# Kernel optimization log

Measured on AMD Instinct MI355X. Metric: run time of the kernel, lower is better.

The kernel has to match this reference:

```python
import jax, jax.numpy as jnp
import numpy as np

CHEB_K = 3  # from init_kwargs

def _layernorm(v, g, b, eps=1e-12):
    mu = jnp.mean(v, axis=-1, keepdims=True)
    var = jnp.var(v, axis=-1, keepdims=True)  # biased, matches torch LayerNorm
    return (v - mu) * jax.lax.rsqrt(var + eps) * g + b

def setup_inputs() -> dict:
    key = jax.random.key(0)
    ks = jax.random.split(key, 5)
    B, N, D_IN, D_OUT, E = 64, 2048, 64, 64, 16
    return {
        "x": jax.random.normal(ks[0], (B, N, D_IN), dtype=jnp.float32),
        "node_embeddings": jax.random.normal(ks[1], (N, E), dtype=jnp.float32),
        "time_embeddings": jax.random.normal(ks[2], (E,), dtype=jnp.float32),
        "weights_pool": jax.random.normal(ks[3], (E, CHEB_K, D_IN, D_OUT), dtype=jnp.float32) * 0.1,
        "bias_pool": jax.random.normal(ks[4], (E, D_OUT), dtype=jnp.float32) * 0.1,
        "ln_gamma": jnp.ones((E,), dtype=jnp.float32),
        "ln_beta": jnp.zeros((E,), dtype=jnp.float32),
    }

def reference(x, node_embeddings, time_embeddings, weights_pool, bias_pool, ln_gamma, ln_beta):
    N = node_embeddings.shape[0]
    # dropout in eval mode -> identity
    ne = _layernorm(node_embeddings + time_embeddings[None, :], ln_gamma, ln_beta)  # [N,E]
    supports0 = jax.nn.softmax(ne @ ne.T, axis=1)  # [N,N]
    support_set = [jnp.eye(N, dtype=x.dtype), supports0]
    for _ in range(2, CHEB_K):
        support_set.append(2.0 * supports0 @ support_set[-1] - support_set[-2])
    supports = jnp.stack(support_set, axis=0)  # [K,N,N]
    weights = jnp.einsum('nd,dkio->nkio', ne, weights_pool)  # [N,K,I,O]
    bias = ne @ bias_pool  # [N,O]
    x_g = jnp.einsum('knm,bmc->bnkc', supports, x)  # [B,N,K,I]
    return jnp.einsum('bnki,nkio->bno', x_g, weights) + bias  # [B,N,O]
```

## Files before the change

### kernel.cpp

```cpp
#include <hip/hip_runtime.h>
#include <stdint.h>

typedef unsigned short u16;
typedef __attribute__((ext_vector_type(8))) short   bf16x8;
typedef __attribute__((ext_vector_type(4))) float   f32x4;
typedef __attribute__((ext_vector_type(4))) u16     u16x4;
typedef __attribute__((ext_vector_type(8))) u16     u16x8;

#define NN 2048
#define BB 64
#define DD 64
#define XSTRIDE (NN*DD)

__device__ __forceinline__ float bf2f(u16 u) {
    union { unsigned int i; float f; } v; v.i = ((unsigned int)u) << 16; return v.f;
}
__device__ __forceinline__ u16 f2bf(float f) {
    union { float f; unsigned int i; } v; v.f = f;
    unsigned int u = v.i;
    return (u16)((u + 0x7fffu + ((u >> 16) & 1u)) >> 16);
}

typedef __attribute__((address_space(3))) unsigned int lds_u32_t;
typedef const __attribute__((address_space(1))) unsigned int g_u32_t;
__device__ __forceinline__ void gload_lds16(const void* g, void* l) {
    __builtin_amdgcn_global_load_lds((g_u32_t*)(uintptr_t)g, (lds_u32_t*)(uintptr_t)l, 16, 0, 0);
}

__global__ __launch_bounds__(256) void k_ln(const float* __restrict__ nodee,
                                            const float* __restrict__ timee,
                                            const float* __restrict__ gamma,
                                            const float* __restrict__ beta,
                                            float* __restrict__ ne,
                                            u16* __restrict__ neb) {
    int n = blockIdx.x * 256 + threadIdx.x;
    float v[16]; float mu = 0.f;
    const float4* p = (const float4*)(nodee + (long)n * 16);
#pragma unroll
    for (int i = 0; i < 4; i++) {
        float4 q = p[i];
        v[i*4+0]=q.x; v[i*4+1]=q.y; v[i*4+2]=q.z; v[i*4+3]=q.w;
    }
#pragma unroll
    for (int e = 0; e < 16; e++) { v[e] += timee[e]; mu += v[e]; }
    mu *= (1.f/16.f);
    float var = 0.f;
#pragma unroll
    for (int e = 0; e < 16; e++) { float d = v[e]-mu; var += d*d; }
    var *= (1.f/16.f);
    float rs = rsqrtf(var + 1e-12f);
    float4* o = (float4*)(ne + (long)n * 16);
    u16x8 nb[2];
#pragma unroll
    for (int i = 0; i < 4; i++) {
        float4 q;
        q.x = (v[i*4+0]-mu)*rs*gamma[i*4+0] + beta[i*4+0];
        q.y = (v[i*4+1]-mu)*rs*gamma[i*4+1] + beta[i*4+1];
        q.z = (v[i*4+2]-mu)*rs*gamma[i*4+2] + beta[i*4+2];
        q.w = (v[i*4+3]-mu)*rs*gamma[i*4+3] + beta[i*4+3];
        o[i] = q;
        nb[i>>1][(i&1)*4+0] = f2bf(q.x); nb[i>>1][(i&1)*4+1] = f2bf(q.y);
        nb[i>>1][(i&1)*4+2] = f2bf(q.z); nb[i>>1][(i&1)*4+3] = f2bf(q.w);
    }
    u16x8 z;
#pragma unroll
    for (int j = 0; j < 8; j++) z[j] = 0;
    u16x8* ob = (u16x8*)&neb[(long)n * 32];
    ob[0] = nb[0]; ob[1] = nb[1]; ob[2] = z; ob[3] = z;
}

__global__ __launch_bounds__(256) void k_wperm(const float* __restrict__ wp,
                                               u16* __restrict__ wpP) {
    int j = blockIdx.x * 256 + threadIdx.x;
    int o = j / 192, ki = j - o * 192;
    int src = ki * 64 + o;
    u16x8 ov[4];
#pragma unroll
    for (int e = 0; e < 16; e++) ov[e>>3][e&7] = f2bf(wp[(long)e*12288 + src]);
#pragma unroll
    for (int e = 0; e < 8; e++) { ov[2][e] = 0; ov[3][e] = 0; }
    u16x8* dst = (u16x8*)&wpP[(long)j * 32];
    dst[0]=ov[0]; dst[1]=ov[1]; dst[2]=ov[2]; dst[3]=ov[3];
}

__global__ __launch_bounds__(256) void k_softmax(const float* __restrict__ ne,
                                                 u16* __restrict__ S) {
    __shared__ float row[2048];
    __shared__ float red[8];
    int n = blockIdx.x, t = threadIdx.x;
    int wave = t >> 6, lane = t & 63;
    f32x4 nev[4];
#pragma unroll
    for (int i = 0; i < 4; i++) nev[i] = *(const f32x4*)&ne[n*16 + i*4];
    float lmax = -1e30f;
    for (int m = t; m < 2048; m += 256) {
        const f32x4* p = (const f32x4*)&ne[m*16];
        f32x4 d4 = nev[0]*p[0] + nev[1]*p[1] + nev[2]*p[2] + nev[3]*p[3];
        float d = d4[0]+d4[1]+d4[2]+d4[3];
        row[m] = d;
        lmax = fmaxf(lmax, d);
    }
#pragma unroll
    for (int off = 32; off > 0; off >>= 1) lmax = fmaxf(lmax, __shfl_xor(lmax, off));
    if (lane == 0) red[wave] = lmax;
    __syncthreads();
    float gmax = fmaxf(fmaxf(red[0], red[1]), fmaxf(red[2], red[3]));
    float lsum = 0.f;
    for (int m = t; m < 2048; m += 256) {
        float ev = __expf(row[m] - gmax);
        row[m] = ev;
        lsum += ev;
    }
#pragma unroll
    for (int off = 32; off > 0; off >>= 1) lsum += __shfl_xor(lsum, off);
    __syncthreads();
    if (lane == 0) red[wave] = lsum;
    __syncthreads();
    float inv = 1.f / (red[0]+red[1]+red[2]+red[3]);
    for (int m = t; m < 2048; m += 256)
        S[(long)n*2048 + m] = f2bf(row[m] * inv);
}

__global__ __launch_bounds__(256) void k_permute(const float* __restrict__ x,
                                                 u16* __restrict__ Xpt) {
    __shared__ u16 T[64][72];
    int bid = blockIdx.x;
    int b = bid >> 5, m0 = (bid & 31) * 64;
    int t = threadIdx.x;
#pragma unroll
    for (int it = 0; it < 4; it++) {
        int fi = it*256 + t;
        int row = fi >> 4, c4 = (fi & 15) * 4;
        float4 v = *(const float4*)&x[(long)b*XSTRIDE + (m0+row)*64 + c4];
        T[c4+0][row] = f2bf(v.x); T[c4+1][row] = f2bf(v.y);
        T[c4+2][row] = f2bf(v.z); T[c4+3][row] = f2bf(v.w);
    }
    __syncthreads();
#pragma unroll
    for (int it = 0; it < 2; it++) {
        int ch = it*256 + t;
        int c = ch >> 3, m8 = (ch & 7) * 8;
        u16x8 v = *(const u16x8*)&T[c][m8];
        *(u16x8*)&Xpt[(long)(b*64 + c)*2048 + m0 + m8] = v;
    }
}

__global__ __launch_bounds__(256) void k_gemm_bt(const u16* __restrict__ A,
                                                 const u16* __restrict__ Bt,
                                                 u16* __restrict__ C,
                                                 int M, int Ncols, int K) {
    __shared__ __align__(16) u16 As[128*32];
    __shared__ __align__(16) u16 Bs[128*32];
    const int t = threadIdx.x;
    const int wave = t >> 6, lane = t & 63;
    const int l15 = lane & 15, lhi = lane >> 4;
    const int m0 = blockIdx.y * 128;
    const int n0 = blockIdx.x * 128;
    const int wr = wave >> 1, wc = wave & 1;
    f32x4 acc[4][4] = {};
    const int srow = t >> 2;
    const int sk = (t & 3) * 8;
    const u16* gA = A + (long)(m0 + srow) * K + sk;
    const u16* gB = Bt + (long)(n0 + srow) * K + sk;
    const long half = (long)64 * K;
    u16* lA = As + wave * 512;
    u16* lB = Bs + wave * 512;
    const int aoff = (wr*64 + l15)*32 + lhi*8;
    const int boff = (wc*64 + l15)*32 + lhi*8;
    for (int k0 = 0; k0 < K; k0 += 32) {
        gload_lds16(gA + k0,        lA);
        gload_lds16(gA + k0 + half, lA + 2048);
        gload_lds16(gB + k0,        lB);
        gload_lds16(gB + k0 + half, lB + 2048);
        __syncthreads();
        bf16x8 af[4], bv[4];
#pragma unroll
        for (int m = 0; m < 4; m++) af[m] = *(const bf16x8*)&As[aoff + m*512];
#pragma unroll
        for (int q = 0; q < 4; q++) bv[q] = *(const bf16x8*)&Bs[boff + q*512];
#pragma unroll
        for (int m = 0; m < 4; m++)
#pragma unroll
            for (int q = 0; q < 4; q++)
                acc[m][q] = __builtin_amdgcn_mfma_f32_16x16x32_bf16(af[m], bv[q], acc[m][q], 0, 0, 0);
        __syncthreads();
    }
#pragma unroll
    for (int m = 0; m < 4; m++) {
        int row = m0 + wr*64 + m*16 + lhi*4;
#pragma unroll
        for (int q = 0; q < 4; q++) {
            int col = n0 + wc*64 + q*16 + l15;
#pragma unroll
            for (int r = 0; r < 4; r++)
                C[(long)(row + r) * Ncols + col] = f2bf(acc[m][q][r]);
        }
    }
}

__global__ __launch_bounds__(512, 1) void k_gemm_big(const u16* __restrict__ A,
                                                     const u16* __restrict__ Bt,
                                                     u16* __restrict__ C,
                                                     int M, int Ncols, int K) {
    __shared__ __align__(16) u16 As0[3 * 128 * 64];
    __shared__ __align__(16) u16 Bs0[3 * 256 * 64];
    const int t = threadIdx.x;
    const int wave = t >> 6, lane = t & 63;
    const int l15 = lane & 15, lhi = lane >> 4;
    const int nwg = gridDim.x * gridDim.y;
    const int wgid = blockIdx.y * gridDim.x + blockIdx.x;
    const int swz = (wgid & 7) * (nwg >> 3) + (wgid >> 3);
    const int by = swz / gridDim.x, bx = swz - (swz / gridDim.x) * gridDim.x;
    const int m0 = by * 128, n0 = bx * 256;
    const int wr = wave >> 2, wc = wave & 3;
    const int NT = K >> 6;
    f32x4 acc[4][4] = {};

    const u16* gAsrc[2];
#pragma unroll
    for (int r = 0; r < 2; r++) {
        int c = r*512 + t, row = c >> 3, slot = c & 7;
        gAsrc[r] = A + (long)(m0 + row) * K + ((slot ^ (row & 7)) * 8);
    }
    const u16* gBsrc[4];
#pragma unroll
    for (int r = 0; r < 4; r++) {
        int c = r*512 + t, row = c >> 3, slot = c & 7;
        gBsrc[r] = Bt + (long)(n0 + row) * K + ((slot ^ (row & 7)) * 8);
    }
    const int ldsA = wave * 512;
    const int ldsB = wave * 512;

    int curA = 0, nxtA = 8192,  tgtA = 16384;
    int curB = 0, nxtB = 16384, tgtB = 32768;

#pragma unroll
    for (int r = 0; r < 2; r++) gload_lds16(gAsrc[r],      &As0[curA + r*4096 + ldsA]);
#pragma unroll
    for (int r = 0; r < 4; r++) gload_lds16(gBsrc[r],      &Bs0[curB + r*4096 + ldsB]);
#pragma unroll
    for (int r = 0; r < 2; r++) gload_lds16(gAsrc[r] + 64, &As0[nxtA + r*4096 + ldsA]);
#pragma unroll
    for (int r = 0; r < 4; r++) gload_lds16(gBsrc[r] + 64, &Bs0[nxtB + r*4096 + ldsB]);
    asm volatile("s_waitcnt vmcnt(6)" ::: "memory");
    __builtin_amdgcn_s_barrier();
    asm volatile("" ::: "memory");

    const int rsw = l15 & 7;
    const int sw0 = (lhi ^ rsw) * 8;
    const int sw1 = ((4 + lhi) ^ rsw) * 8;
    const int aBase = (wr*64 + l15) * 64;
    const int bBase = (wc*64 + l15) * 64;

#pragma unroll 1
    for (int tt = 0; tt < NT; tt++) {
        const bool stg = (tt + 2 < NT);
        const int ko2 = (tt + 2) << 6;
        bf16x8 af0[4], bv0[4];
#pragma unroll
        for (int m = 0; m < 4; m++) af0[m] = *(const bf16x8*)&As0[curA + aBase + m*1024 + sw0];
#pragma unroll
        for (int q = 0; q < 4; q++) bv0[q] = *(const bf16x8*)&Bs0[curB + bBase + q*1024 + sw0];
        if (stg) {
            gload_lds16(gAsrc[0] + ko2, &As0[tgtA + 0*4096 + ldsA]);
            gload_lds16(gAsrc[1] + ko2, &As0[tgtA + 1*4096 + ldsA]);
            gload_lds16(gBsrc[0] + ko2, &Bs0[tgtB + 0*4096 + ldsB]);
        }
        __builtin_amdgcn_s_setprio(1);
#pragma unroll
        for (int m = 0; m < 4; m++)
#pragma unroll
            for (int q = 0; q < 4; q++)
                acc[m][q] = __builtin_amdgcn_mfma_f32_16x16x32_bf16(af0[m], bv0[q], acc[m][q], 0, 0, 0);
        __builtin_amdgcn_s_setprio(0);
        bf16x8 af1[4], bv1[4];
#pragma unroll
        for (int m = 0; m < 4; m++) af1[m] = *(const bf16x8*)&As0[curA + aBase + m*1024 + sw1];
#pragma unroll
        for (int q = 0; q < 4; q++) bv1[q] = *(const bf16x8*)&Bs0[curB + bBase + q*1024 + sw1];
        if (stg) {
            gload_lds16(gBsrc[1] + ko2, &Bs0[tgtB + 1*4096 + ldsB]);
            gload_lds16(gBsrc[2] + ko2, &Bs0[tgtB + 2*4096 + ldsB]);
            gload_lds16(gBsrc[3] + ko2, &Bs0[tgtB + 3*4096 + ldsB]);
        }
        __builtin_amdgcn_s_setprio(1);
#pragma unroll
        for (int m = 0; m < 4; m++)
#pragma unroll
            for (int q = 0; q < 4; q++)
                acc[m][q] = __builtin_amdgcn_mfma_f32_16x16x32_bf16(af1[m], bv1[q], acc[m][q], 0, 0, 0);
        __builtin_amdgcn_s_setprio(0);
        asm volatile("" ::: "memory");
        if (stg)                asm volatile("s_waitcnt vmcnt(6)" ::: "memory");
        else if (tt + 1 < NT)   asm volatile("s_waitcnt vmcnt(0)" ::: "memory");
        if (tt + 1 < NT) {
            __builtin_amdgcn_s_barrier();
            asm volatile("" ::: "memory");
        }
        int ta = curA; curA = nxtA; nxtA = tgtA; tgtA = ta;
        int tb = curB; curB = nxtB; nxtB = tgtB; tgtB = tb;
    }
#pragma unroll
    for (int m = 0; m < 4; m++) {
        int row = m0 + wr*64 + m*16 + lhi*4;
#pragma unroll
        for (int q = 0; q < 4; q++) {
            int col = n0 + wc*64 + q*16 + l15;
#pragma unroll
            for (int r = 0; r < 4; r++)
                C[(long)(row + r) * Ncols + col] = f2bf(acc[m][q][r]);
        }
    }
}

__global__ __launch_bounds__(256) void k_transpose(const u16* __restrict__ in,
                                                   u16* __restrict__ out,
                                                   int R, int Ccols) {
    __shared__ __align__(16) u16 T[64][72];
    int r0 = blockIdx.y * 64, c0 = blockIdx.x * 64;
    int t = threadIdx.x;
#pragma unroll
    for (int it = 0; it < 2; it++) {
        int lin = it*2048 + t*8;
        int r = lin >> 6, c8 = lin & 63;
        u16x8 v = *(const u16x8*)&in[(long)(r0+r)*Ccols + c0 + c8];
        *(u16x8*)&T[r][c8] = v;
    }
    __syncthreads();
#pragma unroll
    for (int it = 0; it < 2; it++) {
        int lin = it*2048 + t*8;
        int c = lin >> 6, r8 = lin & 63;
        u16x8 v;
#pragma unroll
        for (int j = 0; j < 8; j++) v[j] = T[r8+j][c];
        *(u16x8*)&out[(long)(c0+c)*R + r0 + r8] = v;
    }
}

__global__ __launch_bounds__(256) void k_final(const float* __restrict__ x,
                                               const u16* __restrict__ Y1,
                                               const u16* __restrict__ Y2,
                                               const u16* __restrict__ Wt,
                                               const float* __restrict__ ne,
                                               const float* __restrict__ bp,
                                               float* __restrict__ out) {
    __shared__ __align__(16) u16 Al[64*200];
    __shared__ __align__(16) u16 Wl[64*200];
    __shared__ float biasl[64];
    int n = blockIdx.x;
    int t = threadIdx.x;
    int wave = t >> 6, lane = t & 63;
    int l15 = lane & 15, lhi = lane >> 4;
#pragma unroll
    for (int it = 0; it < 6; it++) {
        int ch = it*256 + t;
        int o = ch / 24, kl = (ch % 24) * 8;
        u16x8 v = *(const u16x8*)&Wt[(long)n*12288 + ch*8];
        *(u16x8*)&Wl[o*200 + kl] = v;
    }
    float xs[16];
#pragma unroll
    for (int it = 0; it < 4; it++) {
        int fi = it*256 + t;
        int b = fi >> 4, i4 = (fi & 15) * 4;
        float4 v = *(const float4*)&x[(long)b*XSTRIDE + n*64 + i4];
        xs[it*4+0]=v.x; xs[it*4+1]=v.y; xs[it*4+2]=v.z; xs[it*4+3]=v.w;
        u16x4 p; p[0]=f2bf(v.x); p[1]=f2bf(v.y); p[2]=f2bf(v.z); p[3]=f2bf(v.w);
        *(u16x4*)&Al[b*200 + i4] = p;
    }
#pragma unroll
    for (int it = 0; it < 2; it++) {
        int ch = it*256 + t;
        int b = ch >> 3, i8 = (ch & 7)*8;
        u16x8 v = *(const u16x8*)&Y1[(long)n*4096 + ch*8];
        *(u16x8*)&Al[b*200 + 64 + i8] = v;
    }
#pragma unroll
    for (int it = 0; it < 4; it++) {
        int fi = it*256 + t;
        int b = fi >> 4, i4 = (fi & 15)*4;
        u16x4 y = *(const u16x4*)&Y2[(long)n*4096 + fi*4];
        u16x4 p;
#pragma unroll
        for (int j = 0; j < 4; j++) p[j] = f2bf(2.f*bf2f(y[j]) - xs[it*4+j]);
        *(u16x4*)&Al[b*200 + 128 + i4] = p;
    }
    if (t < 64) {
        float s = 0.f;
#pragma unroll
        for (int e = 0; e < 16; e++) s += ne[n*16+e] * bp[e*64 + t];
        biasl[t] = s;
    }
    __syncthreads();
    f32x4 acc[4] = {};
#pragma unroll
    for (int kk = 0; kk < 6; kk++) {
        bf16x8 bv = *(const bf16x8*)&Wl[(wave*16 + l15)*200 + kk*32 + lhi*8];
#pragma unroll
        for (int m = 0; m < 4; m++) {
            bf16x8 av = *(const bf16x8*)&Al[(m*16 + l15)*200 + kk*32 + lhi*8];
            acc[m] = __builtin_amdgcn_mfma_f32_16x16x32_bf16(av, bv, acc[m], 0, 0, 0);
        }
    }
    int o = wave*16 + l15;
    float bias = biasl[o];
#pragma unroll
    for (int m = 0; m < 4; m++) {
        int brow = m*16 + lhi*4;
#pragma unroll
        for (int r = 0; r < 4; r++)
            out[(long)(brow + r)*XSTRIDE + n*64 + o] = acc[m][r] + bias;
    }
}

extern "C" void kernel_launch(void* const* d_in, const int* in_sizes, int n_in,
                              void* d_out, int out_size, void* d_ws, size_t ws_size,
                              hipStream_t stream) {
    const float* x     = (const float*)d_in[0];
    const float* nodee = (const float*)d_in[1];
    const float* timee = (const float*)d_in[2];
    const float* wp    = (const float*)d_in[3];
    const float* bp    = (const float*)d_in[4];
    const float* gamma = (const float*)d_in[5];
    const float* beta  = (const float*)d_in[6];
    float* out = (float*)d_out;

    char* ws = (char*)d_ws;
    float* ne  = (float*)(ws);
    u16* S     = (u16*)(ws + 131072);
    u16* Xpt   = (u16*)(ws + 8519680);
    u16* Y1    = (u16*)(ws + 25296896);
    u16* Y1t   = (u16*)(ws + 42074112);
    u16* Y2    = (u16*)(ws + 58851328);
    u16* Wt    = (u16*)(ws + 75628544);
    u16* neb   = (u16*)(ws + 58851328);
    u16* wpP   = (u16*)(ws + 58851328 + 131072);
    if (ws_size < (size_t)125960192) return;

    k_ln      <<<8,    256, 0, stream>>>(nodee, timee, gamma, beta, ne, neb);
    k_wperm   <<<48,   256, 0, stream>>>(wp, wpP);
    k_gemm_bt <<<dim3(96,16), 256, 0, stream>>>(neb, wpP, Wt, 2048, 12288, 32);
    k_softmax <<<2048, 256, 0, stream>>>(ne, S);
    k_permute <<<2048, 256, 0, stream>>>(x, Xpt);
    k_gemm_big<<<dim3(16,16), 512, 0, stream>>>(S, Xpt, Y1, 2048, 4096, 2048);
    k_transpose<<<dim3(64,32), 256, 0, stream>>>(Y1, Y1t, 2048, 4096);
    k_gemm_big<<<dim3(16,16), 512, 0, stream>>>(S, Y1t, Y2, 2048, 4096, 2048);
    k_final   <<<2048, 256, 0, stream>>>(x, Y1, Y2, Wt, ne, bp, out);
}
```

Measured before the change: 155.1 us.

## Fuse transpose into GEMM epilogue and switch big GEMM to four waves

The big GEMM goes from 8 waves of 64x64 tiles to 4 waves each computing 64x128, doubling accumulators per wave and reloading operands with the same swizzled LDS layout. The first GEMM also writes a transposed copy of its output through LDS in the epilogue, so the separate transpose kernel and its extra read of Y1 are gone. The intent is to cut a kernel launch plus a memory pass, and to raise MFMA work per LDS read. The cost is much higher register pressure (128 accumulator floats per lane) and fewer waves to hide latency.

```diff
diff --git a/kernel.cpp b/kernel.cpp
--- a/kernel.cpp
+++ b/kernel.cpp
@@ -198,12 +198,12 @@
     }
 }
 
-__global__ __launch_bounds__(512, 1) void k_gemm_big(const u16* __restrict__ A,
+__global__ __launch_bounds__(256, 1) void k_gemm_big(const u16* __restrict__ A,
                                                      const u16* __restrict__ Bt,
                                                      u16* __restrict__ C,
+                                                     u16* __restrict__ Ct,
                                                      int M, int Ncols, int K) {
-    __shared__ __align__(16) u16 As0[3 * 128 * 64];
-    __shared__ __align__(16) u16 Bs0[3 * 256 * 64];
+    __shared__ __align__(16) u16 LB[73728];
     const int t = threadIdx.x;
     const int wave = t >> 6, lane = t & 63;
     const int l15 = lane & 15, lhi = lane >> 4;
@@ -212,86 +212,87 @@
     const int swz = (wgid & 7) * (nwg >> 3) + (wgid >> 3);
     const int by = swz / gridDim.x, bx = swz - (swz / gridDim.x) * gridDim.x;
     const int m0 = by * 128, n0 = bx * 256;
-    const int wr = wave >> 2, wc = wave & 3;
+    const int wr = wave >> 1, wc = wave & 1;
     const int NT = K >> 6;
-    f32x4 acc[4][4] = {};
-
-    const u16* gAsrc[2];
-#pragma unroll
-    for (int r = 0; r < 2; r++) {
-        int c = r*512 + t, row = c >> 3, slot = c & 7;
-        gAsrc[r] = A + (long)(m0 + row) * K + ((slot ^ (row & 7)) * 8);
-    }
-    const u16* gBsrc[4];
-#pragma unroll
-    for (int r = 0; r < 4; r++) {
-        int c = r*512 + t, row = c >> 3, slot = c & 7;
-        gBsrc[r] = Bt + (long)(n0 + row) * K + ((slot ^ (row & 7)) * 8);
-    }
-    const int ldsA = wave * 512;
-    const int ldsB = wave * 512;
-
-    int curA = 0, nxtA = 8192,  tgtA = 16384;
-    int curB = 0, nxtB = 16384, tgtB = 32768;
-
-#pragma unroll
-    for (int r = 0; r < 2; r++) gload_lds16(gAsrc[r],      &As0[curA + r*4096 + ldsA]);
-#pragma unroll
-    for (int r = 0; r < 4; r++) gload_lds16(gBsrc[r],      &Bs0[curB + r*4096 + ldsB]);
-#pragma unroll
-    for (int r = 0; r < 2; r++) gload_lds16(gAsrc[r] + 64, &As0[nxtA + r*4096 + ldsA]);
-#pragma unroll
-    for (int r = 0; r < 4; r++) gload_lds16(gBsrc[r] + 64, &Bs0[nxtB + r*4096 + ldsB]);
-    asm volatile("s_waitcnt vmcnt(6)" ::: "memory");
+    f32x4 acc[4][8] = {};
+
+    const int srow = t >> 3;
+    const int sswz = ((t & 7) ^ (srow & 7)) * 8;
+    const u16* gA0 = A  + (long)(m0 + srow) * K + sswz;
+    const u16* gB0 = Bt + (long)(n0 + srow) * K + sswz;
+    const long rA = (long)32 * K;
+    const int ldsW = wave * 512;
+
+    int curA = 0,     nxtA = 8192,          tgtA = 16384;
+    int curB = 24576, nxtB = 24576 + 16384, tgtB = 24576 + 32768;
+
+#pragma unroll
+    for (int r = 0; r < 4; r++) gload_lds16(gA0 + r*rA,      &LB[curA + r*2048 + ldsW]);
+#pragma unroll
+    for (int r = 0; r < 8; r++) gload_lds16(gB0 + r*rA,      &LB[curB + r*2048 + ldsW]);
+#pragma unroll
+    for (int r = 0; r < 4; r++) gload_lds16(gA0 + r*rA + 64, &LB[nxtA + r*2048 + ldsW]);
+#pragma unroll
+    for (int r = 0; r < 8; r++) gload_lds16(gB0 + r*rA + 64, &LB[nxtB + r*2048 + ldsW]);
+    asm volatile("s_waitcnt vmcnt(12)" ::: "memory");
     __builtin_amdgcn_s_barrier();
     asm volatile("" ::: "memory");
 
-    const int rsw = l15 & 7;
-    const int sw0 = (lhi ^ rsw) * 8;
-    const int sw1 = ((4 + lhi) ^ rsw) * 8;
-    const int aBase = (wr*64 + l15) * 64;
-    const int bBase = (wc*64 + l15) * 64;
+    const int arow = wr*64 + l15, aswz = arow & 7, abase = arow * 64;
+    const int bcol = wc*128 + l15, bswz = bcol & 7, bbase = bcol * 64;
 
 #pragma unroll 1
     for (int tt = 0; tt < NT; tt++) {
         const bool stg = (tt + 2 < NT);
-        const int ko2 = (tt + 2) << 6;
-        bf16x8 af0[4], bv0[4];
-#pragma unroll
-        for (int m = 0; m < 4; m++) af0[m] = *(const bf16x8*)&As0[curA + aBase + m*1024 + sw0];
-#pragma unroll
-        for (int q = 0; q < 4; q++) bv0[q] = *(const bf16x8*)&Bs0[curB + bBase + q*1024 + sw0];
-        if (stg) {
-            gload_lds16(gAsrc[0] + ko2, &As0[tgtA + 0*4096 + ldsA]);
-            gload_lds16(gAsrc[1] + ko2, &As0[tgtA + 1*4096 + ldsA]);
-            gload_lds16(gBsrc[0] + ko2, &Bs0[tgtB + 0*4096 + ldsB]);
-        }
-        __builtin_amdgcn_s_setprio(1);
-#pragma unroll
-        for (int m = 0; m < 4; m++)
-#pragma unroll
-            for (int q = 0; q < 4; q++)
-                acc[m][q] = __builtin_amdgcn_mfma_f32_16x16x32_bf16(af0[m], bv0[q], acc[m][q], 0, 0, 0);
-        __builtin_amdgcn_s_setprio(0);
-        bf16x8 af1[4], bv1[4];
-#pragma unroll
-        for (int m = 0; m < 4; m++) af1[m] = *(const bf16x8*)&As0[curA + aBase + m*1024 + sw1];
-#pragma unroll
-        for (int q = 0; q < 4; q++) bv1[q] = *(const bf16x8*)&Bs0[curB + bBase + q*1024 + sw1];
-        if (stg) {
-            gload_lds16(gBsrc[1] + ko2, &Bs0[tgtB + 1*4096 + ldsB]);
-            gload_lds16(gBsrc[2] + ko2, &Bs0[tgtB + 2*4096 + ldsB]);
-            gload_lds16(gBsrc[3] + ko2, &Bs0[tgtB + 3*4096 + ldsB]);
-        }
-        __builtin_amdgcn_s_setprio(1);
-#pragma unroll
-        for (int m = 0; m < 4; m++)
-#pragma unroll
-            for (int q = 0; q < 4; q++)
-                acc[m][q] = __builtin_amdgcn_mfma_f32_16x16x32_bf16(af1[m], bv1[q], acc[m][q], 0, 0, 0);
-        __builtin_amdgcn_s_setprio(0);
+        const long ko2 = (long)((tt + 2) << 6);
+        {
+            const int sa = (lhi ^ aswz) * 8, sb = (lhi ^ bswz) * 8;
+            bf16x8 af[4], bv[8];
+#pragma unroll
+            for (int m = 0; m < 4; m++) af[m] = *(const bf16x8*)&LB[curA + abase + m*1024 + sa];
+#pragma unroll
+            for (int q = 0; q < 8; q++) bv[q] = *(const bf16x8*)&LB[curB + bbase + q*1024 + sb];
+            if (stg) {
+                gload_lds16(gA0 + 0*rA + ko2, &LB[tgtA + 0*2048 + ldsW]);
+                gload_lds16(gA0 + 1*rA + ko2, &LB[tgtA + 1*2048 + ldsW]);
+                gload_lds16(gA0 + 2*rA + ko2, &LB[tgtA + 2*2048 + ldsW]);
+                gload_lds16(gA0 + 3*rA + ko2, &LB[tgtA + 3*2048 + ldsW]);
+                gload_lds16(gB0 + 0*rA + ko2, &LB[tgtB + 0*2048 + ldsW]);
+                gload_lds16(gB0 + 1*rA + ko2, &LB[tgtB + 1*2048 + ldsW]);
+            }
+            __builtin_amdgcn_s_setprio(1);
+#pragma unroll
+            for (int m = 0; m < 4; m++)
+#pragma unroll
+                for (int q = 0; q < 8; q++)
+                    acc[m][q] = __builtin_amdgcn_mfma_f32_16x16x32_bf16(af[m], bv[q], acc[m][q], 0, 0, 0);
+            __builtin_amdgcn_s_setprio(0);
+        }
+        {
+            const int sa = ((4 + lhi) ^ aswz) * 8, sb = ((4 + lhi) ^ bswz) * 8;
+            bf16x8 af[4], bv[8];
+#pragma unroll
+            for (int m = 0; m < 4; m++) af[m] = *(const bf16x8*)&LB[curA + abase + m*1024 + sa];
+#pragma unroll
+            for (int q = 0; q < 8; q++) bv[q] = *(const bf16x8*)&LB[curB + bbase + q*1024 + sb];
+            if (stg) {
+                gload_lds16(gB0 + 2*rA + ko2, &LB[tgtB + 2*2048 + ldsW]);
+                gload_lds16(gB0 + 3*rA + ko2, &LB[tgtB + 3*2048 + ldsW]);
+                gload_lds16(gB0 + 4*rA + ko2, &LB[tgtB + 4*2048 + ldsW]);
+                gload_lds16(gB0 + 5*rA + ko2, &LB[tgtB + 5*2048 + ldsW]);
+                gload_lds16(gB0 + 6*rA + ko2, &LB[tgtB + 6*2048 + ldsW]);
+                gload_lds16(gB0 + 7*rA + ko2, &LB[tgtB + 7*2048 + ldsW]);
+            }
+            __builtin_amdgcn_s_setprio(1);
+#pragma unroll
+            for (int m = 0; m < 4; m++)
+#pragma unroll
+                for (int q = 0; q < 8; q++)
+                    acc[m][q] = __builtin_amdgcn_mfma_f32_16x16x32_bf16(af[m], bv[q], acc[m][q], 0, 0, 0);
+            __builtin_amdgcn_s_setprio(0);
+        }
         asm volatile("" ::: "memory");
-        if (stg)                asm volatile("s_waitcnt vmcnt(6)" ::: "memory");
+        if (stg)                asm volatile("s_waitcnt vmcnt(12)" ::: "memory");
         else if (tt + 1 < NT)   asm volatile("s_waitcnt vmcnt(0)" ::: "memory");
         if (tt + 1 < NT) {
             __builtin_amdgcn_s_barrier();
@@ -304,37 +305,35 @@
     for (int m = 0; m < 4; m++) {
         int row = m0 + wr*64 + m*16 + lhi*4;
 #pragma unroll
-        for (int q = 0; q < 4; q++) {
-            int col = n0 + wc*64 + q*16 + l15;
+        for (int q = 0; q < 8; q++) {
+            int col = n0 + wc*128 + q*16 + l15;
 #pragma unroll
             for (int r = 0; r < 4; r++)
                 C[(long)(row + r) * Ncols + col] = f2bf(acc[m][q][r]);
         }
     }
-}
-
-__global__ __launch_bounds__(256) void k_transpose(const u16* __restrict__ in,
-                                                   u16* __restrict__ out,
-                                                   int R, int Ccols) {
-    __shared__ __align__(16) u16 T[64][72];
-    int r0 = blockIdx.y * 64, c0 = blockIdx.x * 64;
-    int t = threadIdx.x;
-#pragma unroll
-    for (int it = 0; it < 2; it++) {
-        int lin = it*2048 + t*8;
-        int r = lin >> 6, c8 = lin & 63;
-        u16x8 v = *(const u16x8*)&in[(long)(r0+r)*Ccols + c0 + c8];
-        *(u16x8*)&T[r][c8] = v;
-    }
-    __syncthreads();
-#pragma unroll
-    for (int it = 0; it < 2; it++) {
-        int lin = it*2048 + t*8;
-        int c = lin >> 6, r8 = lin & 63;
-        u16x8 v;
-#pragma unroll
-        for (int j = 0; j < 8; j++) v[j] = T[r8+j][c];
-        *(u16x8*)&out[(long)(c0+c)*R + r0 + r8] = v;
+    if (Ct != nullptr) {
+        __syncthreads();
+#pragma unroll
+        for (int m = 0; m < 4; m++) {
+            int rowb = wr*64 + m*16 + lhi*4;
+#pragma unroll
+            for (int q = 0; q < 8; q++) {
+                int col = wc*128 + q*16 + l15;
+                u16x4 p;
+                p[0]=f2bf(acc[m][q][0]); p[1]=f2bf(acc[m][q][1]);
+                p[2]=f2bf(acc[m][q][2]); p[3]=f2bf(acc[m][q][3]);
+                *(u16x4*)&LB[col*136 + rowb] = p;
+            }
+        }
+        __syncthreads();
+        const int j16 = t >> 4, ch = (t & 15) * 8;
+#pragma unroll
+        for (int p = 0; p < 16; p++) {
+            int j = p*16 + j16;
+            u16x8 v = *(const u16x8*)&LB[j*136 + ch];
+            *(u16x8*)&Ct[(long)(n0 + j)*M + m0 + ch] = v;
+        }
     }
 }
 
@@ -443,8 +442,7 @@
     k_gemm_bt <<<dim3(96,16), 256, 0, stream>>>(neb, wpP, Wt, 2048, 12288, 32);
     k_softmax <<<2048, 256, 0, stream>>>(ne, S);
     k_permute <<<2048, 256, 0, stream>>>(x, Xpt);
-    k_gemm_big<<<dim3(16,16), 512, 0, stream>>>(S, Xpt, Y1, 2048, 4096, 2048);
-    k_transpose<<<dim3(64,32), 256, 0, stream>>>(Y1, Y1t, 2048, 4096);
-    k_gemm_big<<<dim3(16,16), 512, 0, stream>>>(S, Y1t, Y2, 2048, 4096, 2048);
+    k_gemm_big<<<dim3(16,16), 256, 0, stream>>>(S, Xpt, Y1, Y1t, 2048, 4096, 2048);
+    k_gemm_big<<<dim3(16,16), 256, 0, stream>>>(S, Y1t, Y2, (u16*)nullptr, 2048, 4096, 2048);
     k_final   <<<2048, 256, 0, stream>>>(x, Y1, Y2, Wt, ne, bp, out);
 }
```

New measurement: 154.0 us. About the same (-0.7%).
